# Kernel optimization log

Measured on AMD Instinct MI355X. Metric: run time of the kernel, lower is better.

## Reference

```python
import jax, jax.numpy as jnp
import numpy as np

B, S, E, H = 4, 4096, 1024, 128

def setup_inputs() -> dict:
    key = jax.random.key(0)
    kx, kk, kq, kv = jax.random.split(key, 4)
    x = jax.random.normal(kx, (B, S, E), dtype=jnp.float32)
    # torch nn.Linear weights are [out_features, in_features]
    Wk = jax.random.normal(kk, (H, E), dtype=jnp.float32) * (E ** -0.5)
    Wq = jax.random.normal(kq, (H, E), dtype=jnp.float32) * (E ** -0.5)
    Wv = jax.random.normal(kv, (H, E), dtype=jnp.float32) * (E ** -0.5)
    return {"x": x, "Wk": Wk, "Wq": Wq, "Wv": Wv}

def reference(x, Wk, Wq, Wv):
    # projections: y = x @ W.T  (bias-free nn.Linear)
    k = jnp.einsum('bse,he->bsh', x, Wk)
    q = jnp.einsum('bse,he->bsh', x, Wq)
    v = jnp.einsum('bse,he->bsh', x, Wv)
    emb = x.shape[-1]
    # scores scaled by embedding_size**-0.5 (as in the source, not head_size)
    scores = jnp.einsum('bqh,bkh->bqk', q, k) * (emb ** -0.5)  # [B,S,S]
    # causal mask: positions j > i get -inf
    i = jnp.arange(scores.shape[-2])[:, None]
    j = jnp.arange(scores.shape[-1])[None, :]
    scores = jnp.where(j > i, jnp.float32(-jnp.inf), scores)
    probs = jax.nn.softmax(scores, axis=-1)
    # dropout is identity in eval mode
    out = jnp.einsum('bqk,bkh->bqh', probs, v)  # [B,S,H]
    return out
```

## Files before the change

### kernel.cpp

```cpp
#include <hip/hip_runtime.h>

typedef short bf16x8 __attribute__((ext_vector_type(8)));
typedef float f32x4 __attribute__((ext_vector_type(4)));

#define MFMA16(a, b, c) __builtin_amdgcn_mfma_f32_16x16x32_bf16(a, b, c, 0, 0, 0)

constexpr int Bn = 4, Sn = 4096, En = 1024, Hn = 128;
constexpr float CSCALE = 1.44269504089f * 0.03125f;

__device__ inline int sb64(int qt) {
    int a = qt >> 4, r = qt & 15;
    return 8 * a * (a + 1) + r * (a + 1);
}
constexpr int SB = 160;
constexpr int SLOT_F = 8320;

__device__ inline unsigned short f2bf(float f) {
    unsigned int u = __builtin_bit_cast(unsigned int, f);
    u += 0x7fff + ((u >> 16) & 1);
    return (unsigned short)(u >> 16);
}

__device__ inline unsigned int pk2(float a, float b) {
    unsigned int ua = __builtin_bit_cast(unsigned int, a) + 0x8000u;
    unsigned int ub = __builtin_bit_cast(unsigned int, b) + 0x8000u;
    return __builtin_amdgcn_perm(ub, ua, 0x07060302u);
}

__device__ inline void gld16(const unsigned short* g, unsigned short* l) {
    __builtin_amdgcn_global_load_lds((const __attribute__((address_space(1))) void*)g,
                                     (__attribute__((address_space(3))) void*)l, 16, 0, 0);
}

__global__ __launch_bounds__(256) void prep_kernel(
    const float* __restrict__ Wk, const float* __restrict__ Wq, const float* __restrict__ Wv,
    unsigned short* __restrict__ wb)
{
    int gy = blockIdx.x >> 5;
    const float* src = (gy == 0) ? Wq : (gy == 1) ? Wk : Wv;
    unsigned short* dst = wb + (size_t)gy * Hn * En;
    int t = (blockIdx.x & 31) * 256 + threadIdx.x;
    const float4* s4 = (const float4*)src;
    for (int i = 0; i < 4; ++i) {
        float4 v = s4[(size_t)t * 4 + i];
        uint2 w2 = { pk2(v.x, v.y), pk2(v.z, v.w) };
        *(uint2*)&dst[(size_t)t * 16 + i * 4] = w2;
    }
}

__global__ __launch_bounds__(256, 3) void proj_kernel(
    const float* __restrict__ x, const unsigned short* __restrict__ wb,
    unsigned short* __restrict__ qb, unsigned short* __restrict__ kb,
    unsigned short* __restrict__ vbT)
{
    __shared__ __align__(16) unsigned short xs[2][64][64];
    __shared__ __align__(16) unsigned short wsm[2][128][64];

    const int gy = blockIdx.y;
    const unsigned short* wg = wb + (size_t)gy * Hn * En;

    const int m0 = blockIdx.x * 64;
    const int tid = threadIdx.x;
    const int lane = tid & 63, wave = tid >> 6;
    const int l15 = lane & 15, quad = lane >> 4;
    const int wm = (wave & 1) * 32;
    const int wn = (wave >> 1) * 64;

    f32x4 acc[2][4] = {};
    float4 xp[4];

    auto loadx = [&](int kc) {
        for (int p4 = 0; p4 < 4; ++p4) {
            int i = p4 * 256 + tid, row = i >> 4, c4 = (i & 15) * 4;
            xp[p4] = *(const float4*)&x[(size_t)(m0 + row) * En + kc * 64 + c4];
        }
    };
    auto writex = [&](int c) {
        for (int p4 = 0; p4 < 4; ++p4) {
            int i = p4 * 256 + tid, row = i >> 4, hc = i & 15;
            uint2 w2 = { pk2(xp[p4].x, xp[p4].y), pk2(xp[p4].z, xp[p4].w) };
            *(uint2*)((char*)&xs[c][0][0] + row * 128 + (((hc >> 1) ^ (row & 7)) << 4) + ((hc & 1) << 3)) = w2;
        }
    };
    auto issueW = [&](int kc, int c) {
        for (int j = 0; j < 4; ++j) {
            int seg = (wave * 4 + j) * 1024;
            int d = seg + (lane << 4);
            int row = d >> 7, chp = (d >> 4) & 7;
            gld16(wg + (size_t)row * En + kc * 64 + ((chp ^ (row & 7)) << 3),
                  (unsigned short*)((char*)&wsm[c][0][0] + seg));
        }
    };

    loadx(0);
    issueW(0, 0);
    writex(0);
    loadx(1);

    for (int kc = 0; kc < En / 64; ++kc) {
        const int c = kc & 1;
        __syncthreads();
        if (kc + 1 < En / 64) {
            issueW(kc + 1, c ^ 1);
            writex(c ^ 1);
            int kn = (kc + 2 < En / 64) ? kc + 2 : En / 64 - 1;
            loadx(kn);
        }
        bf16x8 xf[2][2], wf[4][2];
        for (int i = 0; i < 2; ++i)
            for (int kk = 0; kk < 2; ++kk) {
                int row = wm + i * 16 + l15;
                int chn = (kk * 4 + quad) ^ (row & 7);
                xf[i][kk] = *(const bf16x8*)((char*)&xs[c][0][0] + row * 128 + (chn << 4));
            }
        for (int j = 0; j < 4; ++j)
            for (int kk = 0; kk < 2; ++kk) {
                int row = wn + j * 16 + l15;
                int chn = (kk * 4 + quad) ^ (row & 7);
                wf[j][kk] = *(const bf16x8*)((char*)&wsm[c][0][0] + row * 128 + (chn << 4));
            }
        if (gy != 2) {
            for (int kk = 0; kk < 2; ++kk)
                for (int i = 0; i < 2; ++i)
                    for (int j = 0; j < 4; ++j)
                        acc[i][j] = MFMA16(xf[i][kk], wf[j][kk], acc[i][j]);
        } else {
            for (int kk = 0; kk < 2; ++kk)
                for (int i = 0; i < 2; ++i)
                    for (int j = 0; j < 4; ++j)
                        acc[i][j] = MFMA16(wf[j][kk], xf[i][kk], acc[i][j]);
        }
    }

    if (gy != 2) {
        unsigned short* ob = (gy == 0) ? qb : kb;
        const float osc = (gy == 0) ? CSCALE : 1.0f;
        for (int i = 0; i < 2; ++i) {
            int rowb = m0 + wm + i * 16 + quad * 4;
            for (int j = 0; j < 4; ++j) {
                int col = wn + j * 16 + l15;
                for (int r = 0; r < 4; ++r)
                    ob[(size_t)(rowb + r) * Hn + col] = f2bf(acc[i][j][r] * osc);
            }
        }
    } else {
        for (int j = 0; j < 4; ++j) {
            int hb = wn + j * 16 + quad * 4;
            for (int i = 0; i < 2; ++i) {
                int sp = m0 + wm + i * 16 + l15;
                int bb = sp >> 12, ss = sp & 4095;
                for (int r = 0; r < 4; ++r)
                    vbT[((size_t)(bb * 128 + hb + r)) * Sn + ss] = f2bf(acc[i][j][r]);
            }
        }
    }
}

__global__ __launch_bounds__(256, 3) void attn_kernel(
    const unsigned short* __restrict__ qb, const unsigned short* __restrict__ kb,
    const unsigned short* __restrict__ vbT, float* __restrict__ out,
    float* __restrict__ part)
{
    __shared__ unsigned short ks[64][132];
    __shared__ unsigned short vt[128][68];
    __shared__ unsigned short ps[4][16][72];

    const int qt = 63 - (int)blockIdx.x;
    const int ch = blockIdx.y;
    const int b  = blockIdx.z;
    const int T  = qt + 1;
    const int nch = (T + 15) >> 4;
    if (ch >= nch) return;
    const int t0 = ch * 16;
    const int nloc = min(16, T - t0);
    const int q0 = qt * 64;

    const int tid = threadIdx.x;
    const int lane = tid & 63, wave = tid >> 6;
    const int l15 = lane & 15, quad = lane >> 4;

    const unsigned short* qg = qb + (size_t)(b * Sn + q0) * Hn;
    bf16x8 qf[4];
    for (int f = 0; f < 4; ++f)
        qf[f] = *(const bf16x8*)&qg[(wave * 16 + l15) * Hn + f * 32 + quad * 8];

    f32x4 o[8] = {};
    float m_r = -INFINITY, l_r = 0.f;

    const unsigned short* kg = kb + (size_t)b * Sn * Hn;
    const unsigned short* vg = vbT + (size_t)b * 128 * Sn;
    unsigned short* psrow = &ps[wave][l15][0];

    bf16x8 kreg[4], vreg[4];
    auto loadKV = [&](int gt) {
        int kt0 = gt * 64;
        for (int p4 = 0; p4 < 4; ++p4) {
            int i = p4 * 256 + tid;
            kreg[p4] = *(const bf16x8*)&kg[(size_t)(kt0 + (i >> 4)) * Hn + (i & 15) * 8];
            vreg[p4] = *(const bf16x8*)&vg[(size_t)(i >> 3) * Sn + kt0 + (i & 7) * 8];
        }
    };

    loadKV(t0);
    for (int tl = 0; tl < nloc; ++tl) {
        const int gt = t0 + tl;
        for (int p4 = 0; p4 < 4; ++p4) {
            int i = p4 * 256 + tid;
            *(bf16x8*)&ks[i >> 4][(i & 15) * 8] = kreg[p4];
            *(bf16x8*)&vt[i >> 3][(i & 7) * 8] = vreg[p4];
        }
        __syncthreads();
        if (tl + 1 < nloc) loadKV(gt + 1);

        float u[4][4];
        for (int nt = 0; nt < 4; ++nt) {
            f32x4 s = {};
            for (int kk = 0; kk < 4; ++kk) {
                bf16x8 kf = *(const bf16x8*)&ks[nt * 16 + l15][kk * 32 + quad * 8];
                s = MFMA16(kf, qf[kk], s);
            }
            for (int r = 0; r < 4; ++r) u[nt][r] = s[r];
        }
        if (gt == qt) {
            int qq = wave * 16 + l15;
            for (int nt = 0; nt < 4; ++nt)
                for (int r = 0; r < 4; ++r)
                    if (nt * 16 + quad * 4 + r > qq) u[nt][r] = -INFINITY;
        }
        float mx = -INFINITY;
        for (int nt = 0; nt < 4; ++nt)
            for (int r = 0; r < 4; ++r) mx = fmaxf(mx, u[nt][r]);
        mx = fmaxf(mx, __shfl_xor(mx, 16));
        mx = fmaxf(mx, __shfl_xor(mx, 32));
        float mn = fmaxf(m_r, mx);
        float alpha = exp2f(m_r - mn);
        m_r = mn;
        float sum = 0.f;
        for (int nt = 0; nt < 4; ++nt)
            for (int r = 0; r < 4; ++r) {
                float pv = exp2f(u[nt][r] - mn);
                u[nt][r] = pv;
                sum += pv;
            }
        sum += __shfl_xor(sum, 16);
        sum += __shfl_xor(sum, 32);
        l_r = l_r * alpha + sum;

        for (int nt = 0; nt < 4; ++nt) {
            uint2 w2 = { pk2(u[nt][0], u[nt][1]), pk2(u[nt][2], u[nt][3]) };
            *(uint2*)&psrow[nt * 16 + quad * 4] = w2;
        }
        for (int t = 0; t < 8; ++t) o[t] *= alpha;

        for (int k2 = 0; k2 < 2; ++k2) {
            bf16x8 pf = *(const bf16x8*)&psrow[k2 * 32 + quad * 8];
            for (int t = 0; t < 8; ++t) {
                bf16x8 vf = *(const bf16x8*)&vt[t * 16 + l15][k2 * 32 + quad * 8];
                o[t] = MFMA16(vf, pf, o[t]);
            }
        }
        __syncthreads();
    }

    if (nch == 1) {
        float inv = 1.0f / l_r;
        float* og = out + (size_t)(b * Sn + q0 + wave * 16 + l15) * Hn;
        for (int t = 0; t < 8; ++t) {
            float4 st = { o[t][0] * inv, o[t][1] * inv, o[t][2] * inv, o[t][3] * inv };
            *(float4*)&og[t * 16 + quad * 4] = st;
        }
    } else {
        float* P = part + (size_t)(b * SB + sb64(qt) + ch) * SLOT_F;
        int q = wave * 16 + l15;
        for (int t = 0; t < 8; ++t) {
            float4 st = { o[t][0], o[t][1], o[t][2], o[t][3] };
            *(float4*)&P[q * 128 + t * 16 + quad * 4] = st;
        }
        if (quad == 0) {
            P[8192 + q] = m_r;
            P[8256 + q] = l_r;
        }
    }
}

__global__ __launch_bounds__(256) void merge_kernel(
    const float* __restrict__ part, float* __restrict__ out)
{
    const int qt = 16 + blockIdx.x;
    const int b = blockIdx.y;
    const int nch = (qt + 16) >> 4;
    const float* P0 = part + (size_t)(b * SB + sb64(qt)) * SLOT_F;
    const int q = threadIdx.x >> 2;
    const int h0 = (threadIdx.x & 3) * 32;

    float m[4], w[4];
    float M = -INFINITY;
    for (int c = 0; c < nch; ++c) {
        m[c] = P0[(size_t)c * SLOT_F + 8192 + q];
        M = fmaxf(M, m[c]);
    }
    float L = 0.f;
    for (int c = 0; c < nch; ++c) {
        w[c] = exp2f(m[c] - M);
        L += w[c] * P0[(size_t)c * SLOT_F + 8256 + q];
    }
    float inv = 1.0f / L;

    float acc[32] = {};
    for (int c = 0; c < nch; ++c) {
        const float* Pq = P0 + (size_t)c * SLOT_F + q * 128 + h0;
        for (int j = 0; j < 8; ++j) {
            float4 v = *(const float4*)&Pq[j * 4];
            acc[j * 4 + 0] += w[c] * v.x;
            acc[j * 4 + 1] += w[c] * v.y;
            acc[j * 4 + 2] += w[c] * v.z;
            acc[j * 4 + 3] += w[c] * v.w;
        }
    }
    float* og = out + (size_t)(b * Sn + qt * 64 + q) * Hn + h0;
    for (int j = 0; j < 8; ++j) {
        float4 st = { acc[j * 4 + 0] * inv, acc[j * 4 + 1] * inv,
                      acc[j * 4 + 2] * inv, acc[j * 4 + 3] * inv };
        *(float4*)&og[j * 4] = st;
    }
}

extern "C" void kernel_launch(void* const* d_in, const int* in_sizes, int n_in,
                              void* d_out, int out_size, void* d_ws, size_t ws_size,
                              hipStream_t stream)
{
    const float* x  = (const float*)d_in[0];
    const float* Wk = (const float*)d_in[1];
    const float* Wq = (const float*)d_in[2];
    const float* Wv = (const float*)d_in[3];
    float* out = (float*)d_out;

    unsigned short* qbuf  = (unsigned short*)d_ws;
    unsigned short* kbuf  = qbuf + (size_t)Bn * Sn * Hn;
    unsigned short* vbufT = kbuf + (size_t)Bn * Sn * Hn;
    unsigned short* wb    = vbufT + (size_t)Bn * Sn * Hn;
    float* part = (float*)(wb + (size_t)3 * Hn * En);

    prep_kernel<<<96, 256, 0, stream>>>(Wk, Wq, Wv, wb);
    proj_kernel<<<dim3(Bn * Sn / 64, 3), 256, 0, stream>>>(x, wb, qbuf, kbuf, vbufT);
    attn_kernel<<<dim3(64, 4, Bn), 256, 0, stream>>>(qbuf, kbuf, vbufT, out, part);
    merge_kernel<<<dim3(48, Bn), 256, 0, stream>>>(part, out);
}
```

Before: 178.3 us.

## Schedule attention work items through a sorted atomic queue with persistent blocks

The prep kernel now builds a work list of (query tile, chunk, batch) items, sorted by descending KV-tile count, in a region of the partials buffer that no partial result uses. The attention kernel becomes persistent: 768 blocks repeatedly claim items with an atomic counter instead of using a fixed 3D grid where many blocks exit early. The aim is longest-first load balancing and no empty blocks, at the cost of an atomic, an extra barrier and a global load per item. Since 768 blocks at 3 per CU may already all be resident, the balancing gain could be small.

```diff
diff --git a/kernel.cpp b/kernel.cpp
--- a/kernel.cpp
+++ b/kernel.cpp
@@ -14,6 +14,7 @@
 }
 constexpr int SB = 160;
 constexpr int SLOT_F = 8320;
+constexpr int NITEMS = 640;
 
 __device__ inline unsigned short f2bf(float f) {
     unsigned int u = __builtin_bit_cast(unsigned int, f);
@@ -34,7 +35,7 @@
 
 __global__ __launch_bounds__(256) void prep_kernel(
     const float* __restrict__ Wk, const float* __restrict__ Wq, const float* __restrict__ Wv,
-    unsigned short* __restrict__ wb)
+    unsigned short* __restrict__ wb, unsigned int* __restrict__ queue)
 {
     int gy = blockIdx.x >> 5;
     const float* src = (gy == 0) ? Wq : (gy == 1) ? Wk : Wv;
@@ -45,6 +46,27 @@
         float4 v = s4[(size_t)t * 4 + i];
         uint2 w2 = { pk2(v.x, v.y), pk2(v.z, v.w) };
         *(uint2*)&dst[(size_t)t * 16 + i * 4] = w2;
+    }
+    if (blockIdx.x == 0) {
+        if (threadIdx.x == 0) queue[0] = 0u;
+        int qt = threadIdx.x >> 2, ch = threadIdx.x & 3;
+        int nch = (qt + 16) >> 4;
+        if (ch < nch) {
+            int nloc = min(16, qt + 1 - ch * 16);
+            int key = (nloc << 6) | qt;
+            int rank = 0;
+            for (int p = 0; p < 256; ++p) {
+                int q2 = p >> 2, c2 = p & 3;
+                int n2 = (q2 + 16) >> 4;
+                if (c2 < n2) {
+                    int nl2 = min(16, q2 + 1 - c2 * 16);
+                    int k2 = (nl2 << 6) | q2;
+                    if (k2 > key || (k2 == key && p < threadIdx.x)) ++rank;
+                }
+            }
+            for (int b = 0; b < 4; ++b)
+                queue[1 + rank * 4 + b] = (unsigned int)(qt | (ch << 6) | (b << 8));
+        }
     }
 }
 
@@ -159,126 +181,133 @@
 __global__ __launch_bounds__(256, 3) void attn_kernel(
     const unsigned short* __restrict__ qb, const unsigned short* __restrict__ kb,
     const unsigned short* __restrict__ vbT, float* __restrict__ out,
-    float* __restrict__ part)
+    float* __restrict__ part, unsigned int* __restrict__ queue)
 {
     __shared__ unsigned short ks[64][132];
     __shared__ unsigned short vt[128][68];
     __shared__ unsigned short ps[4][16][72];
-
-    const int qt = 63 - (int)blockIdx.x;
-    const int ch = blockIdx.y;
-    const int b  = blockIdx.z;
-    const int T  = qt + 1;
-    const int nch = (T + 15) >> 4;
-    if (ch >= nch) return;
-    const int t0 = ch * 16;
-    const int nloc = min(16, T - t0);
-    const int q0 = qt * 64;
+    __shared__ unsigned int sh_item;
 
     const int tid = threadIdx.x;
     const int lane = tid & 63, wave = tid >> 6;
     const int l15 = lane & 15, quad = lane >> 4;
-
-    const unsigned short* qg = qb + (size_t)(b * Sn + q0) * Hn;
-    bf16x8 qf[4];
-    for (int f = 0; f < 4; ++f)
-        qf[f] = *(const bf16x8*)&qg[(wave * 16 + l15) * Hn + f * 32 + quad * 8];
-
-    f32x4 o[8] = {};
-    float m_r = -INFINITY, l_r = 0.f;
-
-    const unsigned short* kg = kb + (size_t)b * Sn * Hn;
-    const unsigned short* vg = vbT + (size_t)b * 128 * Sn;
     unsigned short* psrow = &ps[wave][l15][0];
 
-    bf16x8 kreg[4], vreg[4];
-    auto loadKV = [&](int gt) {
-        int kt0 = gt * 64;
-        for (int p4 = 0; p4 < 4; ++p4) {
-            int i = p4 * 256 + tid;
-            kreg[p4] = *(const bf16x8*)&kg[(size_t)(kt0 + (i >> 4)) * Hn + (i & 15) * 8];
-            vreg[p4] = *(const bf16x8*)&vg[(size_t)(i >> 3) * Sn + kt0 + (i & 7) * 8];
-        }
-    };
-
-    loadKV(t0);
-    for (int tl = 0; tl < nloc; ++tl) {
-        const int gt = t0 + tl;
-        for (int p4 = 0; p4 < 4; ++p4) {
-            int i = p4 * 256 + tid;
-            *(bf16x8*)&ks[i >> 4][(i & 15) * 8] = kreg[p4];
-            *(bf16x8*)&vt[i >> 3][(i & 7) * 8] = vreg[p4];
-        }
+    for (;;) {
+        if (tid == 0) sh_item = atomicAdd(queue, 1u);
         __syncthreads();
-        if (tl + 1 < nloc) loadKV(gt + 1);
-
-        float u[4][4];
-        for (int nt = 0; nt < 4; ++nt) {
-            f32x4 s = {};
-            for (int kk = 0; kk < 4; ++kk) {
-                bf16x8 kf = *(const bf16x8*)&ks[nt * 16 + l15][kk * 32 + quad * 8];
-                s = MFMA16(kf, qf[kk], s);
-            }
-            for (int r = 0; r < 4; ++r) u[nt][r] = s[r];
-        }
-        if (gt == qt) {
-            int qq = wave * 16 + l15;
+        const unsigned int it = sh_item;
+        if (it >= (unsigned int)NITEMS) return;
+        const unsigned int wi = queue[1 + it];
+        const int qt = (int)(wi & 63u);
+        const int ch = (int)((wi >> 6) & 3u);
+        const int b  = (int)((wi >> 8) & 3u);
+        const int T  = qt + 1;
+        const int nch = (T + 15) >> 4;
+        const int t0 = ch * 16;
+        const int nloc = min(16, T - t0);
+        const int q0 = qt * 64;
+
+        const unsigned short* qg = qb + (size_t)(b * Sn + q0) * Hn;
+        bf16x8 qf[4];
+        for (int f = 0; f < 4; ++f)
+            qf[f] = *(const bf16x8*)&qg[(wave * 16 + l15) * Hn + f * 32 + quad * 8];
+
+        f32x4 o[8] = {};
+        float m_r = -INFINITY, l_r = 0.f;
+
+        const unsigned short* kg = kb + (size_t)b * Sn * Hn;
+        const unsigned short* vg = vbT + (size_t)b * 128 * Sn;
+
+        bf16x8 kreg[4], vreg[4];
+        auto loadKV = [&](int gt) {
+            int kt0 = gt * 64;
+            for (int p4 = 0; p4 < 4; ++p4) {
+                int i = p4 * 256 + tid;
+                kreg[p4] = *(const bf16x8*)&kg[(size_t)(kt0 + (i >> 4)) * Hn + (i & 15) * 8];
+                vreg[p4] = *(const bf16x8*)&vg[(size_t)(i >> 3) * Sn + kt0 + (i & 7) * 8];
+            }
+        };
+
+        loadKV(t0);
+        for (int tl = 0; tl < nloc; ++tl) {
+            const int gt = t0 + tl;
+            for (int p4 = 0; p4 < 4; ++p4) {
+                int i = p4 * 256 + tid;
+                *(bf16x8*)&ks[i >> 4][(i & 15) * 8] = kreg[p4];
+                *(bf16x8*)&vt[i >> 3][(i & 7) * 8] = vreg[p4];
+            }
+            __syncthreads();
+            if (tl + 1 < nloc) loadKV(gt + 1);
+
+            float u[4][4];
+            for (int nt = 0; nt < 4; ++nt) {
+                f32x4 s = {};
+                for (int kk = 0; kk < 4; ++kk) {
+                    bf16x8 kf = *(const bf16x8*)&ks[nt * 16 + l15][kk * 32 + quad * 8];
+                    s = MFMA16(kf, qf[kk], s);
+                }
+                for (int r = 0; r < 4; ++r) u[nt][r] = s[r];
+            }
+            if (gt == qt) {
+                int qq = wave * 16 + l15;
+                for (int nt = 0; nt < 4; ++nt)
+                    for (int r = 0; r < 4; ++r)
+                        if (nt * 16 + quad * 4 + r > qq) u[nt][r] = -INFINITY;
+            }
+            float mx = -INFINITY;
             for (int nt = 0; nt < 4; ++nt)
-                for (int r = 0; r < 4; ++r)
-                    if (nt * 16 + quad * 4 + r > qq) u[nt][r] = -INFINITY;
-        }
-        float mx = -INFINITY;
-        for (int nt = 0; nt < 4; ++nt)
-            for (int r = 0; r < 4; ++r) mx = fmaxf(mx, u[nt][r]);
-        mx = fmaxf(mx, __shfl_xor(mx, 16));
-        mx = fmaxf(mx, __shfl_xor(mx, 32));
-        float mn = fmaxf(m_r, mx);
-        float alpha = exp2f(m_r - mn);
-        m_r = mn;
-        float sum = 0.f;
-        for (int nt = 0; nt < 4; ++nt)
-            for (int r = 0; r < 4; ++r) {
-                float pv = exp2f(u[nt][r] - mn);
-                u[nt][r] = pv;
-                sum += pv;
-            }
-        sum += __shfl_xor(sum, 16);
-        sum += __shfl_xor(sum, 32);
-        l_r = l_r * alpha + sum;
-
-        for (int nt = 0; nt < 4; ++nt) {
-            uint2 w2 = { pk2(u[nt][0], u[nt][1]), pk2(u[nt][2], u[nt][3]) };
-            *(uint2*)&psrow[nt * 16 + quad * 4] = w2;
-        }
-        for (int t = 0; t < 8; ++t) o[t] *= alpha;
-
-        for (int k2 = 0; k2 < 2; ++k2) {
-            bf16x8 pf = *(const bf16x8*)&psrow[k2 * 32 + quad * 8];
+                for (int r = 0; r < 4; ++r) mx = fmaxf(mx, u[nt][r]);
+            mx = fmaxf(mx, __shfl_xor(mx, 16));
+            mx = fmaxf(mx, __shfl_xor(mx, 32));
+            float mn = fmaxf(m_r, mx);
+            float alpha = exp2f(m_r - mn);
+            m_r = mn;
+            float sum = 0.f;
+            for (int nt = 0; nt < 4; ++nt)
+                for (int r = 0; r < 4; ++r) {
+                    float pv = exp2f(u[nt][r] - mn);
+                    u[nt][r] = pv;
+                    sum += pv;
+                }
+            sum += __shfl_xor(sum, 16);
+            sum += __shfl_xor(sum, 32);
+            l_r = l_r * alpha + sum;
+
+            for (int nt = 0; nt < 4; ++nt) {
+                uint2 w2 = { pk2(u[nt][0], u[nt][1]), pk2(u[nt][2], u[nt][3]) };
+                *(uint2*)&psrow[nt * 16 + quad * 4] = w2;
+            }
+            for (int t = 0; t < 8; ++t) o[t] *= alpha;
+
+            for (int k2 = 0; k2 < 2; ++k2) {
+                bf16x8 pf = *(const bf16x8*)&psrow[k2 * 32 + quad * 8];
+                for (int t = 0; t < 8; ++t) {
+                    bf16x8 vf = *(const bf16x8*)&vt[t * 16 + l15][k2 * 32 + quad * 8];
+                    o[t] = MFMA16(vf, pf, o[t]);
+                }
+            }
+            __syncthreads();
+        }
+
+        if (nch == 1) {
+            float inv = 1.0f / l_r;
+            float* og = out + (size_t)(b * Sn + q0 + wave * 16 + l15) * Hn;
             for (int t = 0; t < 8; ++t) {
-                bf16x8 vf = *(const bf16x8*)&vt[t * 16 + l15][k2 * 32 + quad * 8];
-                o[t] = MFMA16(vf, pf, o[t]);
-            }
-        }
-        __syncthreads();
-    }
-
-    if (nch == 1) {
-        float inv = 1.0f / l_r;
-        float* og = out + (size_t)(b * Sn + q0 + wave * 16 + l15) * Hn;
-        for (int t = 0; t < 8; ++t) {
-            float4 st = { o[t][0] * inv, o[t][1] * inv, o[t][2] * inv, o[t][3] * inv };
-            *(float4*)&og[t * 16 + quad * 4] = st;
-        }
-    } else {
-        float* P = part + (size_t)(b * SB + sb64(qt) + ch) * SLOT_F;
-        int q = wave * 16 + l15;
-        for (int t = 0; t < 8; ++t) {
-            float4 st = { o[t][0], o[t][1], o[t][2], o[t][3] };
-            *(float4*)&P[q * 128 + t * 16 + quad * 4] = st;
-        }
-        if (quad == 0) {
-            P[8192 + q] = m_r;
-            P[8256 + q] = l_r;
+                float4 st = { o[t][0] * inv, o[t][1] * inv, o[t][2] * inv, o[t][3] * inv };
+                *(float4*)&og[t * 16 + quad * 4] = st;
+            }
+        } else {
+            float* P = part + (size_t)(b * SB + sb64(qt) + ch) * SLOT_F;
+            int q = wave * 16 + l15;
+            for (int t = 0; t < 8; ++t) {
+                float4 st = { o[t][0], o[t][1], o[t][2], o[t][3] };
+                *(float4*)&P[q * 128 + t * 16 + quad * 4] = st;
+            }
+            if (quad == 0) {
+                P[8192 + q] = m_r;
+                P[8256 + q] = l_r;
+            }
         }
     }
 }
@@ -340,9 +369,10 @@
     unsigned short* vbufT = kbuf + (size_t)Bn * Sn * Hn;
     unsigned short* wb    = vbufT + (size_t)Bn * Sn * Hn;
     float* part = (float*)(wb + (size_t)3 * Hn * En);
-
-    prep_kernel<<<96, 256, 0, stream>>>(Wk, Wq, Wv, wb);
+    unsigned int* queue = (unsigned int*)part;
+
+    prep_kernel<<<96, 256, 0, stream>>>(Wk, Wq, Wv, wb, queue);
     proj_kernel<<<dim3(Bn * Sn / 64, 3), 256, 0, stream>>>(x, wb, qbuf, kbuf, vbufT);
-    attn_kernel<<<dim3(64, 4, Bn), 256, 0, stream>>>(qbuf, kbuf, vbufT, out, part);
+    attn_kernel<<<768, 256, 0, stream>>>(qbuf, kbuf, vbufT, out, part, queue);
     merge_kernel<<<dim3(48, Bn), 256, 0, stream>>>(part, out);
 }
```

Measured after the change: 200.5 us. 12.4% more time.

## Launch attention as flat grid driven by precomputed load-balanced work schedule

Applied to the files above, without the earlier changes.

prep_kernel now also fills a 1024-entry table of (query tile, chunk, batch) items. The table packs full 16-tile chunks and the shorter remainder chunks of the causal triangle into four rounds of 256 slots, so each round carries similar work. attn_kernel launches a flat 1024-block grid that reads its item from the table, replacing the old 3D grid where many blocks exited immediately and long and short blocks were unevenly mixed. The goal is less tail imbalance across compute units. The risk is that the table sits at the start of the partials buffer, which attention blocks also write, so a block could read its entry after another block has overwritten it.

```diff
diff --git a/kernel.cpp b/kernel.cpp
--- a/kernel.cpp
+++ b/kernel.cpp
@@ -34,7 +34,7 @@
 
 __global__ __launch_bounds__(256) void prep_kernel(
     const float* __restrict__ Wk, const float* __restrict__ Wq, const float* __restrict__ Wv,
-    unsigned short* __restrict__ wb)
+    unsigned short* __restrict__ wb, unsigned int* __restrict__ sched)
 {
     int gy = blockIdx.x >> 5;
     const float* src = (gy == 0) ? Wq : (gy == 1) ? Wk : Wv;
@@ -45,6 +45,40 @@
         float4 v = s4[(size_t)t * 4 + i];
         uint2 w2 = { pk2(v.x, v.y), pk2(v.z, v.w) };
         *(uint2*)&dst[(size_t)t * 16 + i * 4] = w2;
+    }
+    if (blockIdx.x == 0) {
+        const int bin = threadIdx.x;
+        unsigned int it[4] = { 0xFFFFu, 0xFFFFu, 0xFFFFu, 0xFFFFu };
+        auto fullItem = [](int k) -> unsigned int {
+            int b = k / 100, j = k - 100 * b;
+            int qt = 63, ch = 0;
+            for (int q = 63; q >= 0; --q) {
+                int f = (q + 1) >> 4;
+                if (j < f) { qt = q; ch = j; break; }
+                j -= f;
+            }
+            return (unsigned int)(qt | (ch << 6) | (b << 8));
+        };
+        auto remItem = [](int v, int i) -> unsigned int {
+            int rep = i >> 2, b = i & 3;
+            int qt = rep * 16 + v - 1, ch = rep;
+            return (unsigned int)(qt | (ch << 6) | (b << 8));
+        };
+        if (bin < 128) {
+            it[0] = fullItem(2 * bin);
+            it[1] = fullItem(2 * bin + 1);
+        } else if (bin < 240) {
+            int t2 = bin - 128, v = 2 + (t2 >> 4), i = t2 & 15;
+            it[0] = fullItem(256 + t2);
+            it[1] = remItem(v, i);
+            it[2] = remItem(17 - v, i);
+        } else {
+            int t2 = bin - 240;
+            it[0] = fullItem(368 + 2 * t2);
+            it[1] = fullItem(369 + 2 * t2);
+            it[2] = remItem(1, t2);
+        }
+        for (int z = 0; z < 4; ++z) sched[z * 256 + bin] = it[z];
     }
 }
 
@@ -159,18 +193,19 @@
 __global__ __launch_bounds__(256, 3) void attn_kernel(
     const unsigned short* __restrict__ qb, const unsigned short* __restrict__ kb,
     const unsigned short* __restrict__ vbT, float* __restrict__ out,
-    float* __restrict__ part)
+    float* __restrict__ part, const unsigned int* __restrict__ sched)
 {
     __shared__ unsigned short ks[64][132];
     __shared__ unsigned short vt[128][68];
     __shared__ unsigned short ps[4][16][72];
 
-    const int qt = 63 - (int)blockIdx.x;
-    const int ch = blockIdx.y;
-    const int b  = blockIdx.z;
+    const unsigned int wi = sched[blockIdx.x];
+    if (wi == 0xFFFFu) return;
+    const int qt = (int)(wi & 63u);
+    const int ch = (int)((wi >> 6) & 3u);
+    const int b  = (int)((wi >> 8) & 3u);
     const int T  = qt + 1;
     const int nch = (T + 15) >> 4;
-    if (ch >= nch) return;
     const int t0 = ch * 16;
     const int nloc = min(16, T - t0);
     const int q0 = qt * 64;
@@ -340,9 +375,10 @@
     unsigned short* vbufT = kbuf + (size_t)Bn * Sn * Hn;
     unsigned short* wb    = vbufT + (size_t)Bn * Sn * Hn;
     float* part = (float*)(wb + (size_t)3 * Hn * En);
-
-    prep_kernel<<<96, 256, 0, stream>>>(Wk, Wq, Wv, wb);
+    unsigned int* sched = (unsigned int*)part;
+
+    prep_kernel<<<96, 256, 0, stream>>>(Wk, Wq, Wv, wb, sched);
     proj_kernel<<<dim3(Bn * Sn / 64, 3), 256, 0, stream>>>(x, wb, qbuf, kbuf, vbufT);
-    attn_kernel<<<dim3(64, 4, Bn), 256, 0, stream>>>(qbuf, kbuf, vbufT, out, part);
+    attn_kernel<<<1024, 256, 0, stream>>>(qbuf, kbuf, vbufT, out, part, sched);
     merge_kernel<<<dim3(48, Bn), 256, 0, stream>>>(part, out);
 }
```

Result: faster. 174.4 us (-2.2%).

## Process 128-row query tiles per attention block with a precomputed longest-first schedule

Applied to the files above, without the earlier changes.

The attention kernel now handles 128 query rows per block, with each wave running two 16-row groups, so every K/V tile staged in shared memory feeds twice as many MFMAs. This halves the K/V global and LDS traffic per query row. prep_kernel also builds a work list of (query tile, chunk, batch) items sorted by chunk length, longest first. attn_kernel launches exactly that many blocks, so there are no empty early-exit blocks and the long tiles start first. Partial-result slots and the merge kernel are resized for 128-row tiles; the cost is higher register pressure, with occupancy lowered to 2 blocks per CU.

```diff
diff --git a/kernel.cpp b/kernel.cpp
--- a/kernel.cpp
+++ b/kernel.cpp
@@ -8,12 +8,12 @@
 constexpr int Bn = 4, Sn = 4096, En = 1024, Hn = 128;
 constexpr float CSCALE = 1.44269504089f * 0.03125f;
 
-__device__ inline int sb64(int qt) {
-    int a = qt >> 4, r = qt & 15;
-    return 8 * a * (a + 1) + r * (a + 1);
-}
-constexpr int SB = 160;
-constexpr int SLOT_F = 8320;
+__device__ inline int sbase(int qt2) {
+    int a = qt2 >> 3, r = qt2 & 7;
+    return (a + 1) * (4 * a + r);
+}
+constexpr int SLOT2_F = 16640;
+constexpr int NIT = 320;
 
 __device__ inline unsigned short f2bf(float f) {
     unsigned int u = __builtin_bit_cast(unsigned int, f);
@@ -34,7 +34,7 @@
 
 __global__ __launch_bounds__(256) void prep_kernel(
     const float* __restrict__ Wk, const float* __restrict__ Wq, const float* __restrict__ Wv,
-    unsigned short* __restrict__ wb)
+    unsigned short* __restrict__ wb, unsigned int* __restrict__ sched)
 {
     int gy = blockIdx.x >> 5;
     const float* src = (gy == 0) ? Wq : (gy == 1) ? Wk : Wv;
@@ -45,6 +45,31 @@
         float4 v = s4[(size_t)t * 4 + i];
         uint2 w2 = { pk2(v.x, v.y), pk2(v.z, v.w) };
         *(uint2*)&dst[(size_t)t * 16 + i * 4] = w2;
+    }
+    if (blockIdx.x == 0 && threadIdx.x < 80) {
+        const int p = threadIdx.x;
+        int qt2 = 0, ch = 0, acc = 0;
+        for (int q = 0; q < 32; ++q) {
+            int n = (q >> 3) + 1;
+            if (p < acc + n) { qt2 = q; ch = p - acc; break; }
+            acc += n;
+        }
+        int nloc = min(16, 2 * qt2 + 2 - 16 * ch);
+        int key = nloc * 64 + qt2;
+        int rank = 0;
+        for (int p2 = 0; p2 < 80; ++p2) {
+            int q2 = 0, c2 = 0, a2 = 0;
+            for (int q = 0; q < 32; ++q) {
+                int n = (q >> 3) + 1;
+                if (p2 < a2 + n) { q2 = q; c2 = p2 - a2; break; }
+                a2 += n;
+            }
+            int nl2 = min(16, 2 * q2 + 2 - 16 * c2);
+            int k2 = nl2 * 64 + q2;
+            if (k2 > key || (k2 == key && p2 < p)) ++rank;
+        }
+        for (int b = 0; b < 4; ++b)
+            sched[rank * 4 + b] = (unsigned int)(qt2 | (ch << 6) | (b << 8));
     }
 }
 
@@ -156,40 +181,40 @@
     }
 }
 
-__global__ __launch_bounds__(256, 3) void attn_kernel(
+__global__ __launch_bounds__(256, 2) void attn_kernel(
     const unsigned short* __restrict__ qb, const unsigned short* __restrict__ kb,
     const unsigned short* __restrict__ vbT, float* __restrict__ out,
-    float* __restrict__ part)
+    float* __restrict__ part, const unsigned int* __restrict__ sched)
 {
     __shared__ unsigned short ks[64][132];
     __shared__ unsigned short vt[128][68];
-    __shared__ unsigned short ps[4][16][72];
-
-    const int qt = 63 - (int)blockIdx.x;
-    const int ch = blockIdx.y;
-    const int b  = blockIdx.z;
-    const int T  = qt + 1;
-    const int nch = (T + 15) >> 4;
-    if (ch >= nch) return;
+    __shared__ unsigned short ps[4][32][72];
+
+    const unsigned int wi = sched[blockIdx.x];
+    const int qt2 = (int)(wi & 63u);
+    const int ch  = (int)((wi >> 6) & 3u);
+    const int b   = (int)((wi >> 8) & 3u);
+    const int T2  = 2 * qt2 + 2;
+    const int nch = (qt2 >> 3) + 1;
     const int t0 = ch * 16;
-    const int nloc = min(16, T - t0);
-    const int q0 = qt * 64;
+    const int nloc = min(16, T2 - t0);
+    const int q0 = qt2 * 128;
 
     const int tid = threadIdx.x;
     const int lane = tid & 63, wave = tid >> 6;
     const int l15 = lane & 15, quad = lane >> 4;
 
     const unsigned short* qg = qb + (size_t)(b * Sn + q0) * Hn;
-    bf16x8 qf[4];
-    for (int f = 0; f < 4; ++f)
-        qf[f] = *(const bf16x8*)&qg[(wave * 16 + l15) * Hn + f * 32 + quad * 8];
-
-    f32x4 o[8] = {};
-    float m_r = -INFINITY, l_r = 0.f;
+    bf16x8 qf[2][4];
+    for (int g = 0; g < 2; ++g)
+        for (int f = 0; f < 4; ++f)
+            qf[g][f] = *(const bf16x8*)&qg[(wave * 32 + g * 16 + l15) * Hn + f * 32 + quad * 8];
+
+    f32x4 o[2][8] = {};
+    float m_r[2] = { -INFINITY, -INFINITY }, l_r[2] = { 0.f, 0.f };
 
     const unsigned short* kg = kb + (size_t)b * Sn * Hn;
     const unsigned short* vg = vbT + (size_t)b * 128 * Sn;
-    unsigned short* psrow = &ps[wave][l15][0];
 
     bf16x8 kreg[4], vreg[4];
     auto loadKV = [&](int gt) {
@@ -212,73 +237,86 @@
         __syncthreads();
         if (tl + 1 < nloc) loadKV(gt + 1);
 
-        float u[4][4];
+        float u[2][4][4];
         for (int nt = 0; nt < 4; ++nt) {
-            f32x4 s = {};
+            f32x4 s0 = {}, s1 = {};
             for (int kk = 0; kk < 4; ++kk) {
                 bf16x8 kf = *(const bf16x8*)&ks[nt * 16 + l15][kk * 32 + quad * 8];
-                s = MFMA16(kf, qf[kk], s);
-            }
-            for (int r = 0; r < 4; ++r) u[nt][r] = s[r];
-        }
-        if (gt == qt) {
-            int qq = wave * 16 + l15;
+                s0 = MFMA16(kf, qf[0][kk], s0);
+                s1 = MFMA16(kf, qf[1][kk], s1);
+            }
+            for (int r = 0; r < 4; ++r) { u[0][nt][r] = s0[r]; u[1][nt][r] = s1[r]; }
+        }
+        if (gt >= 2 * qt2) {
+            int kof = (gt - 2 * qt2) * 64;
+            for (int g = 0; g < 2; ++g) {
+                int qq = wave * 32 + g * 16 + l15;
+                for (int nt = 0; nt < 4; ++nt)
+                    for (int r = 0; r < 4; ++r)
+                        if (kof + nt * 16 + quad * 4 + r > qq) u[g][nt][r] = -INFINITY;
+            }
+        }
+        for (int g = 0; g < 2; ++g) {
+            float mx = -INFINITY;
             for (int nt = 0; nt < 4; ++nt)
-                for (int r = 0; r < 4; ++r)
-                    if (nt * 16 + quad * 4 + r > qq) u[nt][r] = -INFINITY;
-        }
-        float mx = -INFINITY;
-        for (int nt = 0; nt < 4; ++nt)
-            for (int r = 0; r < 4; ++r) mx = fmaxf(mx, u[nt][r]);
-        mx = fmaxf(mx, __shfl_xor(mx, 16));
-        mx = fmaxf(mx, __shfl_xor(mx, 32));
-        float mn = fmaxf(m_r, mx);
-        float alpha = exp2f(m_r - mn);
-        m_r = mn;
-        float sum = 0.f;
-        for (int nt = 0; nt < 4; ++nt)
-            for (int r = 0; r < 4; ++r) {
-                float pv = exp2f(u[nt][r] - mn);
-                u[nt][r] = pv;
-                sum += pv;
-            }
-        sum += __shfl_xor(sum, 16);
-        sum += __shfl_xor(sum, 32);
-        l_r = l_r * alpha + sum;
-
-        for (int nt = 0; nt < 4; ++nt) {
-            uint2 w2 = { pk2(u[nt][0], u[nt][1]), pk2(u[nt][2], u[nt][3]) };
-            *(uint2*)&psrow[nt * 16 + quad * 4] = w2;
-        }
-        for (int t = 0; t < 8; ++t) o[t] *= alpha;
+                for (int r = 0; r < 4; ++r) mx = fmaxf(mx, u[g][nt][r]);
+            mx = fmaxf(mx, __shfl_xor(mx, 16));
+            mx = fmaxf(mx, __shfl_xor(mx, 32));
+            float mn = fmaxf(m_r[g], mx);
+            float alpha = exp2f(m_r[g] - mn);
+            m_r[g] = mn;
+            float sum = 0.f;
+            for (int nt = 0; nt < 4; ++nt)
+                for (int r = 0; r < 4; ++r) {
+                    float pv = exp2f(u[g][nt][r] - mn);
+                    u[g][nt][r] = pv;
+                    sum += pv;
+                }
+            sum += __shfl_xor(sum, 16);
+            sum += __shfl_xor(sum, 32);
+            l_r[g] = l_r[g] * alpha + sum;
+
+            unsigned short* psrow = &ps[wave][g * 16 + l15][0];
+            for (int nt = 0; nt < 4; ++nt) {
+                uint2 w2 = { pk2(u[g][nt][0], u[g][nt][1]), pk2(u[g][nt][2], u[g][nt][3]) };
+                *(uint2*)&psrow[nt * 16 + quad * 4] = w2;
+            }
+            for (int t = 0; t < 8; ++t) o[g][t] *= alpha;
+        }
 
         for (int k2 = 0; k2 < 2; ++k2) {
-            bf16x8 pf = *(const bf16x8*)&psrow[k2 * 32 + quad * 8];
+            bf16x8 pf0 = *(const bf16x8*)&ps[wave][0 * 16 + l15][k2 * 32 + quad * 8];
+            bf16x8 pf1 = *(const bf16x8*)&ps[wave][1 * 16 + l15][k2 * 32 + quad * 8];
             for (int t = 0; t < 8; ++t) {
                 bf16x8 vf = *(const bf16x8*)&vt[t * 16 + l15][k2 * 32 + quad * 8];
-                o[t] = MFMA16(vf, pf, o[t]);
+                o[0][t] = MFMA16(vf, pf0, o[0][t]);
+                o[1][t] = MFMA16(vf, pf1, o[1][t]);
             }
         }
         __syncthreads();
     }
 
     if (nch == 1) {
-        float inv = 1.0f / l_r;
-        float* og = out + (size_t)(b * Sn + q0 + wave * 16 + l15) * Hn;
-        for (int t = 0; t < 8; ++t) {
-            float4 st = { o[t][0] * inv, o[t][1] * inv, o[t][2] * inv, o[t][3] * inv };
-            *(float4*)&og[t * 16 + quad * 4] = st;
+        for (int g = 0; g < 2; ++g) {
+            float inv = 1.0f / l_r[g];
+            float* og = out + (size_t)(b * Sn + q0 + wave * 32 + g * 16 + l15) * Hn;
+            for (int t = 0; t < 8; ++t) {
+                float4 st = { o[g][t][0] * inv, o[g][t][1] * inv, o[g][t][2] * inv, o[g][t][3] * inv };
+                *(float4*)&og[t * 16 + quad * 4] = st;
+            }
         }
     } else {
-        float* P = part + (size_t)(b * SB + sb64(qt) + ch) * SLOT_F;
-        int q = wave * 16 + l15;
-        for (int t = 0; t < 8; ++t) {
-            float4 st = { o[t][0], o[t][1], o[t][2], o[t][3] };
-            *(float4*)&P[q * 128 + t * 16 + quad * 4] = st;
-        }
-        if (quad == 0) {
-            P[8192 + q] = m_r;
-            P[8256 + q] = l_r;
+        float* P = part + (size_t)(b * 80 + sbase(qt2) + ch) * SLOT2_F;
+        for (int g = 0; g < 2; ++g) {
+            int q = wave * 32 + g * 16 + l15;
+            for (int t = 0; t < 8; ++t) {
+                float4 st = { o[g][t][0], o[g][t][1], o[g][t][2], o[g][t][3] };
+                *(float4*)&P[q * 128 + t * 16 + quad * 4] = st;
+            }
+            if (quad == 0) {
+                P[16384 + q] = m_r[g];
+                P[16512 + q] = l_r[g];
+            }
         }
     }
 }
@@ -286,29 +324,30 @@
 __global__ __launch_bounds__(256) void merge_kernel(
     const float* __restrict__ part, float* __restrict__ out)
 {
-    const int qt = 16 + blockIdx.x;
+    const int qt2 = 8 + (blockIdx.x >> 1);
+    const int half = blockIdx.x & 1;
     const int b = blockIdx.y;
-    const int nch = (qt + 16) >> 4;
-    const float* P0 = part + (size_t)(b * SB + sb64(qt)) * SLOT_F;
-    const int q = threadIdx.x >> 2;
+    const int nch = (qt2 >> 3) + 1;
+    const float* P0 = part + (size_t)(b * 80 + sbase(qt2)) * SLOT2_F;
+    const int q = half * 64 + (threadIdx.x >> 2);
     const int h0 = (threadIdx.x & 3) * 32;
 
     float m[4], w[4];
     float M = -INFINITY;
     for (int c = 0; c < nch; ++c) {
-        m[c] = P0[(size_t)c * SLOT_F + 8192 + q];
+        m[c] = P0[(size_t)c * SLOT2_F + 16384 + q];
         M = fmaxf(M, m[c]);
     }
     float L = 0.f;
     for (int c = 0; c < nch; ++c) {
         w[c] = exp2f(m[c] - M);
-        L += w[c] * P0[(size_t)c * SLOT_F + 8256 + q];
+        L += w[c] * P0[(size_t)c * SLOT2_F + 16512 + q];
     }
     float inv = 1.0f / L;
 
     float acc[32] = {};
     for (int c = 0; c < nch; ++c) {
-        const float* Pq = P0 + (size_t)c * SLOT_F + q * 128 + h0;
+        const float* Pq = P0 + (size_t)c * SLOT2_F + q * 128 + h0;
         for (int j = 0; j < 8; ++j) {
             float4 v = *(const float4*)&Pq[j * 4];
             acc[j * 4 + 0] += w[c] * v.x;
@@ -317,7 +356,7 @@
             acc[j * 4 + 3] += w[c] * v.w;
         }
     }
-    float* og = out + (size_t)(b * Sn + qt * 64 + q) * Hn + h0;
+    float* og = out + (size_t)(b * Sn + qt2 * 128 + q) * Hn + h0;
     for (int j = 0; j < 8; ++j) {
         float4 st = { acc[j * 4 + 0] * inv, acc[j * 4 + 1] * inv,
                       acc[j * 4 + 2] * inv, acc[j * 4 + 3] * inv };
@@ -340,9 +379,10 @@
     unsigned short* vbufT = kbuf + (size_t)Bn * Sn * Hn;
     unsigned short* wb    = vbufT + (size_t)Bn * Sn * Hn;
     float* part = (float*)(wb + (size_t)3 * Hn * En);
-
-    prep_kernel<<<96, 256, 0, stream>>>(Wk, Wq, Wv, wb);
+    unsigned int* sched = (unsigned int*)part;
+
+    prep_kernel<<<96, 256, 0, stream>>>(Wk, Wq, Wv, wb, sched);
     proj_kernel<<<dim3(Bn * Sn / 64, 3), 256, 0, stream>>>(x, wb, qbuf, kbuf, vbufT);
-    attn_kernel<<<dim3(64, 4, Bn), 256, 0, stream>>>(qbuf, kbuf, vbufT, out, part);
+    attn_kernel<<<NIT, 256, 0, stream>>>(qbuf, kbuf, vbufT, out, part, sched);
     merge_kernel<<<dim3(48, Bn), 256, 0, stream>>>(part, out);
 }
```

New measurement: 186.8 us. 4.8% more time.
